# Optimization experiments

Measured on AMD Instinct MI355X. Metric: run time of the kernel, lower is better.

The kernel has to match this reference:

```python
import jax, jax.numpy as jnp
import numpy as np

B, S, D = 8, 2048, 512
H, LAT, OUT = 8, 64, 64


def setup_inputs() -> dict:
    key = jax.random.key(0)
    ks = jax.random.split(key, 5)
    return {
        "x": jax.random.normal(ks[0], (B, S, D), dtype=jnp.float32),
        "WQ": jax.random.normal(ks[1], (H, D, LAT), dtype=jnp.float32) * 0.05,
        "WK": jax.random.normal(ks[2], (H, D, LAT), dtype=jnp.float32) * 0.05,
        "WV": jax.random.normal(ks[3], (H, D, OUT), dtype=jnp.float32) * 0.05,
        "WO": jax.random.normal(ks[4], (H * OUT, OUT), dtype=jnp.float32) * 0.05,
    }


def reference(x, WQ, WK, WV, WO):
    # Per-head projections, vectorized over heads (faithful to the TF python loop).
    Q = jnp.einsum('bsd,hdk->bhsk', x, WQ)   # [B,H,S,LAT]
    K = jnp.einsum('bsd,hdk->bhsk', x, WK)   # [B,H,S,LAT]
    V = jnp.einsum('bsd,hdo->bhso', x, WV)   # [B,H,S,OUT]
    scale = jnp.asarray(1.0 / np.sqrt(LAT), dtype=x.dtype)
    A = jnp.einsum('bhqk,bhsk->bhqs', Q, K) * scale  # [B,H,S,S]
    A = jax.nn.softmax(A, axis=-1)
    O = jnp.einsum('bhqs,bhso->bhqo', A, V)  # [B,H,S,OUT]
    # concat heads along last axis (head 0 first, matching the TF loop order)
    O = jnp.transpose(O, (0, 2, 1, 3)).reshape(x.shape[0], x.shape[1], H * OUT)
    return O @ WO  # [B,S,OUT]
```

## Files before the change

kernel.cpp:

```cpp
#include <hip/hip_runtime.h>
#include <hip/hip_bf16.h>
#include <math.h>

static constexpr int Bn = 8, Sn = 2048, Dn = 512, Hn = 8, LATn = 64, OUTn = 64;

typedef short  bf16x8 __attribute__((ext_vector_type(8)));
typedef float  f32x4  __attribute__((ext_vector_type(4)));

__device__ __forceinline__ unsigned short f2bf(float f) {
    union { float f; unsigned int i; } v; v.f = f;
    unsigned int x = v.i;
    return (unsigned short)((x + 0x7FFFu + ((x >> 16) & 1u)) >> 16);
}
__device__ __forceinline__ unsigned int pack2bf(float a, float b) {
    unsigned int ua = __float_as_uint(a) + 0x8000u;
    unsigned int ub = __float_as_uint(b) + 0x8000u;
    return (ua >> 16) | (ub & 0xFFFF0000u);
}
__device__ __forceinline__ unsigned int cvtpk(float a, float b) {
    unsigned int r;
    asm("v_cvt_pk_bf16_f32 %0, %1, %2" : "=v"(r) : "v"(a), "v"(b));
    return r;
}

#if __has_builtin(__builtin_amdgcn_exp2f)
#define EXP2(x) __builtin_amdgcn_exp2f(x)
#else
#define EXP2(x) exp2f(x)
#endif

__device__ __forceinline__ void gl_lds16(const void* g, void* l) {
    __builtin_amdgcn_global_load_lds(
        (const __attribute__((address_space(1))) unsigned int*)g,
        (__attribute__((address_space(3))) unsigned int*)l, 16, 0, 0);
}

__global__ __launch_bounds__(256) void xprep(
    const float* __restrict__ x, unsigned short* __restrict__ Xb)
{
    const size_t base = ((size_t)blockIdx.x * 256 + threadIdx.x) * 16;
    const float* src = x + base;
    float4 u0 = *(const float4*)(src);
    float4 u1 = *(const float4*)(src + 4);
    float4 u2 = *(const float4*)(src + 8);
    float4 u3 = *(const float4*)(src + 12);
    unsigned int pk[8] = { pack2bf(u0.x,u0.y), pack2bf(u0.z,u0.w),
                           pack2bf(u1.x,u1.y), pack2bf(u1.z,u1.w),
                           pack2bf(u2.x,u2.y), pack2bf(u2.z,u2.w),
                           pack2bf(u3.x,u3.y), pack2bf(u3.z,u3.w) };
    *(bf16x8*)(Xb + base)     = *(bf16x8*)(pk);
    *(bf16x8*)(Xb + base + 8) = *(bf16x8*)(pk + 4);
}

__global__ __launch_bounds__(256) void wprep(
    const float* __restrict__ WQ, const float* __restrict__ WK,
    const float* __restrict__ WV, const float* __restrict__ WO,
    unsigned short* __restrict__ WT)
{
    __shared__ float tile[64][65];
    const int t  = threadIdx.x;
    const int d0 = blockIdx.x * 64;
    const int yy = blockIdx.y;

    const float* W; float scale = 1.0f; size_t dstbase;
    if (yy < 24) {
        int h = yy / 3, which = yy % 3;
        W = (which == 0) ? WQ : (which == 1) ? WK : WV;
        W += (size_t)h * Dn * 64;
        if (which == 0) scale = 0.125f * 1.44269504088896f;
        dstbase = ((size_t)h * 192 + which * 64) * Dn;
    } else {
        W = WO;
        dstbase = (size_t)8 * 192 * Dn;
    }

    for (int i = 0; i < 4; ++i) {
        int idx = i * 256 + t;
        int r = idx >> 4, c = (idx & 15) * 4;
        float4 u = *(const float4*)(W + (size_t)(d0 + r) * 64 + c);
        tile[r][c] = u.x; tile[r][c+1] = u.y; tile[r][c+2] = u.z; tile[r][c+3] = u.w;
    }
    __syncthreads();
    const int n = t & 63, dd = t >> 6;
    unsigned short pk[16];
    for (int i = 0; i < 16; ++i) pk[i] = f2bf(tile[dd*16 + i][n] * scale);
    size_t dst = dstbase + (size_t)n * Dn + d0 + dd * 16;
    *(bf16x8*)(WT + dst)     = *(bf16x8*)(pk);
    *(bf16x8*)(WT + dst + 8) = *(bf16x8*)(pk + 8);
}

__global__ __launch_bounds__(256, 4) void qkv_mfma(
    const unsigned short* __restrict__ Xb, const unsigned short* __restrict__ WT,
    unsigned short* __restrict__ Qb, unsigned short* __restrict__ Kb,
    unsigned short* __restrict__ VT)
{
    __shared__ __align__(16) unsigned short lds[64 * 200];
    unsigned short* L = lds;

    const int t  = threadIdx.x;
    const int w  = t >> 6, ln = t & 63;
    const int nl = ln & 15, g = ln >> 4;
    const int bh = blockIdx.y, b = bh >> 3, h = bh & 7;
    const int s0 = blockIdx.x * 64;

    const int r0 = t >> 3,      sc0 = (t & 7) ^ (r0 & 7);
    const int r1 = 32 + (t>>3), sc1 = (t & 7) ^ (r1 & 7);
    const unsigned short* xg0 = Xb + ((size_t)(b * Sn + s0 + r0)) * Dn + sc0 * 8;
    const unsigned short* xg1 = Xb + ((size_t)(b * Sn + s0 + r1)) * Dn + sc1 * 8;

    const int p = nl & 7;
    const int aoff0 = nl * 64 + 8 * ((g    ) ^ p);
    const int aoff1 = nl * 64 + 8 * ((4 + g) ^ p);

    const unsigned short* wb = WT + ((size_t)h * 192 + 48 * w + nl) * Dn + 8 * g;

    f32x4 acc[4][3];
    for (int m = 0; m < 4; ++m)
        for (int j = 0; j < 3; ++j) acc[m][j] = (f32x4){0.f, 0.f, 0.f, 0.f};

    gl_lds16(xg0, lds + 512 * w);
    gl_lds16(xg1, lds + 2048 + 512 * w);
    bf16x8 wv[3][2];
    #pragma unroll
    for (int j = 0; j < 3; ++j) {
        wv[j][0] = *(const bf16x8*)(wb + j * 8192);
        wv[j][1] = *(const bf16x8*)(wb + j * 8192 + 32);
    }

    #pragma unroll
    for (int kt = 0; kt < 8; ++kt) {
        asm volatile("s_waitcnt vmcnt(0)" ::: "memory");
        __builtin_amdgcn_s_barrier();
        bf16x8 wn[3][2];
        if (kt < 7) {
            unsigned short* dst = lds + 4096 * ((kt + 1) & 1);
            gl_lds16(xg0 + (kt + 1) * 64, dst + 512 * w);
            gl_lds16(xg1 + (kt + 1) * 64, dst + 2048 + 512 * w);
            #pragma unroll
            for (int j = 0; j < 3; ++j) {
                wn[j][0] = *(const bf16x8*)(wb + j * 8192 + (kt + 1) * 64);
                wn[j][1] = *(const bf16x8*)(wb + j * 8192 + (kt + 1) * 64 + 32);
            }
        }
        const unsigned short* cur = lds + 4096 * (kt & 1);

        #pragma unroll
        for (int kc = 0; kc < 2; ++kc) {
            bf16x8 a[4];
            #pragma unroll
            for (int m = 0; m < 4; ++m)
                a[m] = *(const bf16x8*)(cur + (kc ? aoff1 : aoff0) + m * 1024);
            #pragma unroll
            for (int m = 0; m < 4; ++m)
                #pragma unroll
                for (int j = 0; j < 3; ++j)
                    acc[m][j] = __builtin_amdgcn_mfma_f32_16x16x32_bf16(
                                    a[m], wv[j][kc], acc[m][j], 0, 0, 0);
        }
        if (kt < 7) {
            #pragma unroll
            for (int j = 0; j < 3; ++j) {
                wv[j][0] = wn[j][0];
                wv[j][1] = wn[j][1];
            }
        }
    }
    __syncthreads();
    for (int m = 0; m < 4; ++m)
        for (int j = 0; j < 3; ++j) {
            int n = 48*w + 16*j + nl;
            for (int r = 0; r < 4; ++r)
                L[(16*m + 4*g + r)*200 + n] = f2bf(acc[m][j][r]);
        }
    __syncthreads();
    for (int i = 0; i < 4; ++i) {
        int idx = i * 256 + t;
        int r = idx >> 4, c = (idx & 15) * 8;
        bf16x8 v = *(const bf16x8*)(L + r*200 + c);
        size_t o = ((size_t)bh * Sn + s0 + r) * 64;
        if (c < 64) *(bf16x8*)(Qb + o + c)      = v;
        else        *(bf16x8*)(Kb + o + c - 64) = v;
    }
    {
        int o = t & 63, cc = t >> 6;
        unsigned short pk[16];
        for (int i = 0; i < 16; ++i) {
            int srow = 32*(cc>>1) + 16*((i>>2)&1) + 8*(cc&1) + 4*((i>>3)&1) + (i&3);
            pk[i] = L[srow*200 + 128 + o];
        }
        size_t dst = ((size_t)bh * 64 + o) * Sn + s0 + 16*cc;
        *(bf16x8*)(VT + dst)     = *(bf16x8*)(pk);
        *(bf16x8*)(VT + dst + 8) = *(bf16x8*)(pk + 8);
    }
}

__global__ __launch_bounds__(512, 4) void flash_mfma(
    const unsigned short* __restrict__ Qb,
    const unsigned short* __restrict__ Kb,
    const unsigned short* __restrict__ VT,
    unsigned short* __restrict__ Ob)
{
    __shared__ __align__(16) unsigned short KV[3][2][4096];

    const int t  = threadIdx.x;
    const int w  = t >> 6, ln = t & 63;
    const int qh = ln & 15, g = (ln >> 4) & 3;
    const int bh = blockIdx.y, b = bh >> 3, h = bh & 7;
    const int q0 = blockIdx.x * 256;
    const int qw = q0 + 32 * w;

    bf16x8 bq[2][2];
    #pragma unroll
    for (int qs = 0; qs < 2; ++qs) {
        const unsigned short* qp =
            Qb + ((size_t)bh * Sn + qw + 16*qs + qh) * 64 + 8*g;
        bq[qs][0] = *(const bf16x8*)(qp);
        bq[qs][1] = *(const bf16x8*)(qp + 32);
    }

    const int r0 = t >> 3;
    const int cs = (t & 7) ^ (r0 & 7);
    const unsigned short* kg = Kb + ((size_t)bh * Sn + r0) * 64 + cs * 8;
    const unsigned short* vg = VT + ((size_t)bh * 64 + r0) * Sn + cs * 8;

    const int koff0 = qh*64 + (((g    ) ^ (qh & 7)) * 8);
    const int koff1 = qh*64 + (((4 + g) ^ (qh & 7)) * 8);

    f32x4 o_acc[2][4];
    #pragma unroll
    for (int qs = 0; qs < 2; ++qs)
        #pragma unroll
        for (int f = 0; f < 4; ++f) o_acc[qs][f] = (f32x4){0.f, 0.f, 0.f, 0.f};
    float l_run[2] = {0.f, 0.f};

    gl_lds16(kg,        &KV[0][0][w * 512]);
    gl_lds16(vg,        &KV[0][1][w * 512]);
    gl_lds16(kg + 4096, &KV[1][0][w * 512]);
    gl_lds16(vg + 64,   &KV[1][1][w * 512]);

    constexpr int NT = Sn / 64;
    int buf = 0, sbuf = 2;
    for (int kt = 0; kt < NT; ++kt) {
        if (kt < NT - 1) asm volatile("s_waitcnt vmcnt(2)" ::: "memory");
        else             asm volatile("s_waitcnt vmcnt(0)" ::: "memory");
        __builtin_amdgcn_s_barrier();

        if (kt < NT - 2) {
            gl_lds16(kg + (size_t)(kt + 2) * 4096, &KV[sbuf][0][w * 512]);
            gl_lds16(vg + (size_t)(kt + 2) * 64,   &KV[sbuf][1][w * 512]);
        }
        const unsigned short* Kt = KV[buf][0];
        const unsigned short* Vt = KV[buf][1];

        f32x4 st[2][4];
        #pragma unroll
        for (int qs = 0; qs < 2; ++qs)
            #pragma unroll
            for (int f = 0; f < 4; ++f) st[qs][f] = (f32x4){0.f, 0.f, 0.f, 0.f};
        __builtin_amdgcn_s_setprio(1);
        #pragma unroll
        for (int kc = 0; kc < 2; ++kc) {
            const int ko = kc ? koff1 : koff0;
            bf16x8 a0 = *(const bf16x8*)(Kt + ko);
            bf16x8 a1 = *(const bf16x8*)(Kt + ko + 1024);
            bf16x8 a2 = *(const bf16x8*)(Kt + ko + 2048);
            bf16x8 a3 = *(const bf16x8*)(Kt + ko + 3072);
            #pragma unroll
            for (int qs = 0; qs < 2; ++qs) {
                st[qs][0] = __builtin_amdgcn_mfma_f32_16x16x32_bf16(a0, bq[qs][kc], st[qs][0], 0, 0, 0);
                st[qs][1] = __builtin_amdgcn_mfma_f32_16x16x32_bf16(a1, bq[qs][kc], st[qs][1], 0, 0, 0);
                st[qs][2] = __builtin_amdgcn_mfma_f32_16x16x32_bf16(a2, bq[qs][kc], st[qs][2], 0, 0, 0);
                st[qs][3] = __builtin_amdgcn_mfma_f32_16x16x32_bf16(a3, bq[qs][kc], st[qs][3], 0, 0, 0);
            }
        }
        __builtin_amdgcn_s_setprio(0);

        bf16x8 bp[2][2];
        #pragma unroll
        for (int qs = 0; qs < 2; ++qs) {
            float e0[4], e1[4], e2[4], e3[4];
            #pragma unroll
            for (int r = 0; r < 4; ++r) {
                e0[r] = EXP2(st[qs][0][r]);
                e1[r] = EXP2(st[qs][1][r]);
                e2[r] = EXP2(st[qs][2][r]);
                e3[r] = EXP2(st[qs][3][r]);
            }
            l_run[qs] += ((e0[0]+e0[1])+(e0[2]+e0[3])) + ((e1[0]+e1[1])+(e1[2]+e1[3]))
                       + ((e2[0]+e2[1])+(e2[2]+e2[3])) + ((e3[0]+e3[1])+(e3[2]+e3[3]));
            unsigned int p0[4] = { cvtpk(e0[0],e0[1]), cvtpk(e0[2],e0[3]),
                                   cvtpk(e1[0],e1[1]), cvtpk(e1[2],e1[3]) };
            unsigned int p1[4] = { cvtpk(e2[0],e2[1]), cvtpk(e2[2],e2[3]),
                                   cvtpk(e3[0],e3[1]), cvtpk(e3[2],e3[3]) };
            bp[qs][0] = *(bf16x8*)p0;
            bp[qs][1] = *(bf16x8*)p1;
        }

        __builtin_amdgcn_s_setprio(1);
        #pragma unroll
        for (int kc = 0; kc < 2; ++kc) {
            const int ko = kc ? koff1 : koff0;
            bf16x8 v0 = *(const bf16x8*)(Vt + ko);
            bf16x8 v1 = *(const bf16x8*)(Vt + ko + 1024);
            bf16x8 v2 = *(const bf16x8*)(Vt + ko + 2048);
            bf16x8 v3 = *(const bf16x8*)(Vt + ko + 3072);
            #pragma unroll
            for (int qs = 0; qs < 2; ++qs) {
                o_acc[qs][0] = __builtin_amdgcn_mfma_f32_16x16x32_bf16(v0, bp[qs][kc], o_acc[qs][0], 0, 0, 0);
                o_acc[qs][1] = __builtin_amdgcn_mfma_f32_16x16x32_bf16(v1, bp[qs][kc], o_acc[qs][1], 0, 0, 0);
                o_acc[qs][2] = __builtin_amdgcn_mfma_f32_16x16x32_bf16(v2, bp[qs][kc], o_acc[qs][2], 0, 0, 0);
                o_acc[qs][3] = __builtin_amdgcn_mfma_f32_16x16x32_bf16(v3, bp[qs][kc], o_acc[qs][3], 0, 0, 0);
            }
        }
        __builtin_amdgcn_s_setprio(0);

        buf  = (buf  == 2) ? 0 : buf  + 1;
        sbuf = (sbuf == 2) ? 0 : sbuf + 1;
    }

    #pragma unroll
    for (int qs = 0; qs < 2; ++qs) {
        l_run[qs] += __shfl_xor(l_run[qs], 16);
        l_run[qs] += __shfl_xor(l_run[qs], 32);
    }

    #pragma unroll
    for (int qs = 0; qs < 2; ++qs) {
        float inv_l = 1.f / l_run[qs];
        unsigned short* op = Ob
            + ((size_t)(b * Sn + q0 + 32*w + 16*qs + qh)) * 512 + h*64 + 4*g;
        #pragma unroll
        for (int f = 0; f < 4; ++f) {
            unsigned int lo = cvtpk(o_acc[qs][f][0] * inv_l, o_acc[qs][f][1] * inv_l);
            unsigned int hi = cvtpk(o_acc[qs][f][2] * inv_l, o_acc[qs][f][3] * inv_l);
            *(uint2*)(op + 16*f) = make_uint2(lo, hi);
        }
    }
}

__global__ __launch_bounds__(256) void out_mfma(
    const unsigned short* __restrict__ Ob, const unsigned short* __restrict__ WOT,
    float* __restrict__ out)
{
    __shared__ __align__(16) unsigned short As[64 * 72];
    __shared__ __align__(16) unsigned short Bs[64 * 72];

    const int t  = threadIdx.x;
    const int w  = t >> 6, ln = t & 63;
    const int qh = ln & 15, g = ln >> 4;
    const int bs0 = blockIdx.x * 64;

    f32x4 acc[4];
    for (int n = 0; n < 4; ++n) acc[n] = (f32x4){0.f, 0.f, 0.f, 0.f};

    for (int k0 = 0; k0 < 512; k0 += 64) {
        __syncthreads();
        for (int i = 0; i < 2; ++i) {
            int idx = i * 256 + t;
            int r = idx >> 3, c = (idx & 7) * 8;
            *(bf16x8*)(As + r*72 + c) =
                *(const bf16x8*)(Ob + ((size_t)(bs0 + r)) * 512 + k0 + c);
            *(bf16x8*)(Bs + r*72 + c) =
                *(const bf16x8*)(WOT + (size_t)r * Dn + k0 + c);
        }
        __syncthreads();
        #pragma unroll
        for (int kc = 0; kc < 2; ++kc) {
            bf16x8 a = *(const bf16x8*)(As + (16*w + qh)*72 + 32*kc + 8*g);
            #pragma unroll
            for (int n = 0; n < 4; ++n) {
                bf16x8 bb = *(const bf16x8*)(Bs + (16*n + qh)*72 + 32*kc + 8*g);
                acc[n] = __builtin_amdgcn_mfma_f32_16x16x32_bf16(a, bb, acc[n], 0, 0, 0);
            }
        }
    }
    for (int n = 0; n < 4; ++n)
        for (int r = 0; r < 4; ++r)
            out[((size_t)(bs0 + 16*w + 4*g + r)) * 64 + 16*n + qh] = acc[n][r];
}

extern "C" void kernel_launch(void* const* d_in, const int* in_sizes, int n_in,
                              void* d_out, int out_size, void* d_ws, size_t ws_size,
                              hipStream_t stream)
{
    const float* x  = (const float*)d_in[0];
    const float* WQ = (const float*)d_in[1];
    const float* WK = (const float*)d_in[2];
    const float* WV = (const float*)d_in[3];
    const float* WO = (const float*)d_in[4];
    float* out = (float*)d_out;

    const size_t NQ = (size_t)Bn * Hn * Sn * LATn;
    char* p = (char*)d_ws;
    unsigned short* Qb  = (unsigned short*)p;           p += NQ * 2;
    unsigned short* Kb  = (unsigned short*)p;           p += NQ * 2;
    unsigned short* VT  = (unsigned short*)p;           p += NQ * 2;
    unsigned short* WT  = (unsigned short*)p;           p += ((size_t)Hn*192*Dn + 64*Dn) * 2;
    unsigned short* Ob  = (unsigned short*)p;
    unsigned short* WOT = WT + (size_t)Hn * 192 * Dn;
    unsigned short* Xb  = Ob;

    xprep     <<<dim3(2048),          256, 0, stream>>>(x, Xb);
    wprep     <<<dim3(8, 25),         256, 0, stream>>>(WQ, WK, WV, WO, WT);
    qkv_mfma  <<<dim3(Sn/64, Bn*Hn),  256, 0, stream>>>(Xb, WT, Qb, Kb, VT);
    flash_mfma<<<dim3(Sn/256, Bn*Hn), 512, 0, stream>>>(Qb, Kb, VT, Ob);
    out_mfma  <<<dim3(Bn*Sn/64),      256, 0, stream>>>(Ob, WOT, out);
}
```

Baseline: 212.4 us.

## Merge prep kernels, remap QKV grid, and triple-buffer output GEMM loads

Folds the x-conversion and weight-transpose kernels into one launch, which removes a kernel launch and the gap between them. The QKV projection grid becomes 1D with a swizzled block-to-tile mapping, and its launch-bounds occupancy hint drops from 4 to 3. The output projection now loads tiles with async global-to-LDS copies into a 3-stage ring buffer with XOR swizzling, replacing the padded synchronous loads. These changes aim to cut launch overhead and hide memory latency, at the cost of more LDS per block in the output GEMM and possibly lower occupancy in the QKV kernel.

```diff
diff --git a/kernel.cpp b/kernel.cpp
--- a/kernel.cpp
+++ b/kernel.cpp
@@ -35,32 +35,35 @@
         (__attribute__((address_space(3))) unsigned int*)l, 16, 0, 0);
 }
 
-__global__ __launch_bounds__(256) void xprep(
-    const float* __restrict__ x, unsigned short* __restrict__ Xb)
-{
-    const size_t base = ((size_t)blockIdx.x * 256 + threadIdx.x) * 16;
-    const float* src = x + base;
-    float4 u0 = *(const float4*)(src);
-    float4 u1 = *(const float4*)(src + 4);
-    float4 u2 = *(const float4*)(src + 8);
-    float4 u3 = *(const float4*)(src + 12);
-    unsigned int pk[8] = { pack2bf(u0.x,u0.y), pack2bf(u0.z,u0.w),
-                           pack2bf(u1.x,u1.y), pack2bf(u1.z,u1.w),
-                           pack2bf(u2.x,u2.y), pack2bf(u2.z,u2.w),
-                           pack2bf(u3.x,u3.y), pack2bf(u3.z,u3.w) };
-    *(bf16x8*)(Xb + base)     = *(bf16x8*)(pk);
-    *(bf16x8*)(Xb + base + 8) = *(bf16x8*)(pk + 4);
-}
-
-__global__ __launch_bounds__(256) void wprep(
+__global__ __launch_bounds__(256) void prep(
+    const float* __restrict__ x,
     const float* __restrict__ WQ, const float* __restrict__ WK,
     const float* __restrict__ WV, const float* __restrict__ WO,
-    unsigned short* __restrict__ WT)
+    unsigned short* __restrict__ Xb, unsigned short* __restrict__ WT)
 {
     __shared__ float tile[64][65];
+    const int id = blockIdx.x;
     const int t  = threadIdx.x;
-    const int d0 = blockIdx.x * 64;
-    const int yy = blockIdx.y;
+
+    if (id < 2048) {
+        const size_t base = ((size_t)id * 256 + t) * 16;
+        const float* src = x + base;
+        float4 u0 = *(const float4*)(src);
+        float4 u1 = *(const float4*)(src + 4);
+        float4 u2 = *(const float4*)(src + 8);
+        float4 u3 = *(const float4*)(src + 12);
+        unsigned int pk[8] = { pack2bf(u0.x,u0.y), pack2bf(u0.z,u0.w),
+                               pack2bf(u1.x,u1.y), pack2bf(u1.z,u1.w),
+                               pack2bf(u2.x,u2.y), pack2bf(u2.z,u2.w),
+                               pack2bf(u3.x,u3.y), pack2bf(u3.z,u3.w) };
+        *(bf16x8*)(Xb + base)     = *(bf16x8*)(pk);
+        *(bf16x8*)(Xb + base + 8) = *(bf16x8*)(pk + 4);
+        return;
+    }
+
+    const int rem = id - 2048;
+    const int d0 = (rem & 7) * 64;
+    const int yy = rem >> 3;
 
     const float* W; float scale = 1.0f; size_t dstbase;
     if (yy < 24) {
@@ -89,7 +92,7 @@
     *(bf16x8*)(WT + dst + 8) = *(bf16x8*)(pk + 8);
 }
 
-__global__ __launch_bounds__(256, 4) void qkv_mfma(
+__global__ __launch_bounds__(256, 3) void qkv_mfma(
     const unsigned short* __restrict__ Xb, const unsigned short* __restrict__ WT,
     unsigned short* __restrict__ Qb, unsigned short* __restrict__ Kb,
     unsigned short* __restrict__ VT)
@@ -100,8 +103,9 @@
     const int t  = threadIdx.x;
     const int w  = t >> 6, ln = t & 63;
     const int nl = ln & 15, g = ln >> 4;
-    const int bh = blockIdx.y, b = bh >> 3, h = bh & 7;
-    const int s0 = blockIdx.x * 64;
+    const int logical = (blockIdx.x & 7) * 256 + (blockIdx.x >> 3);
+    const int s0 = (logical & 31) * 64;
+    const int bh = logical >> 5, b = bh >> 3, h = bh & 7;
 
     const int r0 = t >> 3,      sc0 = (t & 7) ^ (r0 & 7);
     const int r1 = 32 + (t>>3), sc1 = (t & 7) ^ (r1 & 7);
@@ -342,37 +346,65 @@
     const unsigned short* __restrict__ Ob, const unsigned short* __restrict__ WOT,
     float* __restrict__ out)
 {
-    __shared__ __align__(16) unsigned short As[64 * 72];
-    __shared__ __align__(16) unsigned short Bs[64 * 72];
+    __shared__ __align__(16) unsigned short AB[3][2][4096];
 
     const int t  = threadIdx.x;
     const int w  = t >> 6, ln = t & 63;
     const int qh = ln & 15, g = ln >> 4;
     const int bs0 = blockIdx.x * 64;
 
+    const int r0 = t >> 3,      cs0 = (t & 7) ^ (r0 & 7);
+    const int r1 = 32 + (t>>3), cs1 = (t & 7) ^ (r1 & 7);
+    const unsigned short* ag0 = Ob + ((size_t)(bs0 + r0)) * 512 + cs0 * 8;
+    const unsigned short* ag1 = Ob + ((size_t)(bs0 + r1)) * 512 + cs1 * 8;
+    const unsigned short* bg0 = WOT + (size_t)r0 * Dn + cs0 * 8;
+    const unsigned short* bg1 = WOT + (size_t)r1 * Dn + cs1 * 8;
+
+    const int foff0 = qh*64 + 8 * (((    g) ^ (qh & 7)));
+    const int foff1 = qh*64 + 8 * (((4 + g) ^ (qh & 7)));
+
     f32x4 acc[4];
     for (int n = 0; n < 4; ++n) acc[n] = (f32x4){0.f, 0.f, 0.f, 0.f};
 
-    for (int k0 = 0; k0 < 512; k0 += 64) {
-        __syncthreads();
-        for (int i = 0; i < 2; ++i) {
-            int idx = i * 256 + t;
-            int r = idx >> 3, c = (idx & 7) * 8;
-            *(bf16x8*)(As + r*72 + c) =
-                *(const bf16x8*)(Ob + ((size_t)(bs0 + r)) * 512 + k0 + c);
-            *(bf16x8*)(Bs + r*72 + c) =
-                *(const bf16x8*)(WOT + (size_t)r * Dn + k0 + c);
-        }
-        __syncthreads();
+    gl_lds16(ag0,      &AB[0][0][w * 512]);
+    gl_lds16(ag1,      &AB[0][0][2048 + w * 512]);
+    gl_lds16(bg0,      &AB[0][1][w * 512]);
+    gl_lds16(bg1,      &AB[0][1][2048 + w * 512]);
+    gl_lds16(ag0 + 64, &AB[1][0][w * 512]);
+    gl_lds16(ag1 + 64, &AB[1][0][2048 + w * 512]);
+    gl_lds16(bg0 + 64, &AB[1][1][w * 512]);
+    gl_lds16(bg1 + 64, &AB[1][1][2048 + w * 512]);
+
+    constexpr int NT = 8;
+    int buf = 0, sbuf = 2;
+    for (int kt = 0; kt < NT; ++kt) {
+        if (kt < NT - 1) asm volatile("s_waitcnt vmcnt(4)" ::: "memory");
+        else             asm volatile("s_waitcnt vmcnt(0)" ::: "memory");
+        __builtin_amdgcn_s_barrier();
+
+        if (kt < NT - 2) {
+            const int ko = (kt + 2) * 64;
+            gl_lds16(ag0 + ko, &AB[sbuf][0][w * 512]);
+            gl_lds16(ag1 + ko, &AB[sbuf][0][2048 + w * 512]);
+            gl_lds16(bg0 + ko, &AB[sbuf][1][w * 512]);
+            gl_lds16(bg1 + ko, &AB[sbuf][1][2048 + w * 512]);
+        }
+        const unsigned short* At = AB[buf][0];
+        const unsigned short* Bt = AB[buf][1];
+
         #pragma unroll
         for (int kc = 0; kc < 2; ++kc) {
-            bf16x8 a = *(const bf16x8*)(As + (16*w + qh)*72 + 32*kc + 8*g);
+            const int fo = kc ? foff1 : foff0;
+            bf16x8 a = *(const bf16x8*)(At + fo + w * 1024);
             #pragma unroll
             for (int n = 0; n < 4; ++n) {
-                bf16x8 bb = *(const bf16x8*)(Bs + (16*n + qh)*72 + 32*kc + 8*g);
+                bf16x8 bb = *(const bf16x8*)(Bt + fo + n * 1024);
                 acc[n] = __builtin_amdgcn_mfma_f32_16x16x32_bf16(a, bb, acc[n], 0, 0, 0);
             }
         }
+
+        buf  = (buf  == 2) ? 0 : buf  + 1;
+        sbuf = (sbuf == 2) ? 0 : sbuf + 1;
     }
     for (int n = 0; n < 4; ++n)
         for (int r = 0; r < 4; ++r)
@@ -400,9 +432,8 @@
     unsigned short* WOT = WT + (size_t)Hn * 192 * Dn;
     unsigned short* Xb  = Ob;
 
-    xprep     <<<dim3(2048),          256, 0, stream>>>(x, Xb);
-    wprep     <<<dim3(8, 25),         256, 0, stream>>>(WQ, WK, WV, WO, WT);
-    qkv_mfma  <<<dim3(Sn/64, Bn*Hn),  256, 0, stream>>>(Xb, WT, Qb, Kb, VT);
+    prep      <<<dim3(2248),          256, 0, stream>>>(x, WQ, WK, WV, WO, Xb, WT);
+    qkv_mfma  <<<dim3(2048),          256, 0, stream>>>(Xb, WT, Qb, Kb, VT);
     flash_mfma<<<dim3(Sn/256, Bn*Hn), 512, 0, stream>>>(Qb, Kb, VT, Ob);
     out_mfma  <<<dim3(Bn*Sn/64),      256, 0, stream>>>(Ob, WOT, out);
 }
```

After: 212.0 us. No clear change (-0.2%).
